# Kernel optimization log

Measured on AMD Instinct MI355X. Metric: run time of the kernel, lower is better.

## Reference

```python
import jax, jax.numpy as jnp
import numpy as np

N_GROUPS = 4


def setup_inputs() -> dict:
    key = jax.random.key(0)
    k1, k2 = jax.random.split(key)
    x = jax.random.normal(k1, (64, 256, 32, 32), dtype=jnp.float32)
    # codebook: (group_size, num_embeddings) = (256 // 4, 512), torch.rand init
    weight = jax.random.uniform(k2, (64, 512), dtype=jnp.float32)
    return {"x": x, "weight": weight}


def _group_quantize(xg, emb):
    # xg: (B, g, H, W), emb: (g, K)
    # squared Euclidean distance; argmin is identical to argmin of torch.norm
    d2 = (jnp.sum(xg * xg, axis=1)[..., None]
          - 2.0 * jnp.einsum('bghw,gk->bhwk', xg, emb)
          + jnp.sum(emb * emb, axis=0))        # (B, H, W, K)
    argmin = jnp.argmin(d2, axis=-1)            # (B, H, W)
    result = jnp.transpose(emb.T[argmin], (0, 3, 1, 2))  # (B, g, H, W)
    return result, argmin


def reference(x, weight):
    B, D, H, W = x.shape
    g = D // N_GROUPS
    results = []
    argmins = []
    for i in range(N_GROUPS):  # fixed small structural loop
        r, a = _group_quantize(x[:, i * g:(i + 1) * g], weight)
        results.append(r)
        argmins.append(a)
    result = jnp.concatenate(results, axis=1) / jnp.sqrt(jnp.float32(N_GROUPS))
    argmins = jnp.stack(argmins, axis=1)  # (B, n_groups, H, W)
    return result, argmins
```

## Files before the change

kernel.cpp:

```cpp
#include <hip/hip_runtime.h>
#include <float.h>

#define KCODES 512
#define GDIM 64
#define TAU 4.0e-3f

typedef __attribute__((ext_vector_type(8))) short short8;
typedef __attribute__((ext_vector_type(4))) float floatx4;


__device__ __forceinline__ void bf16split(float x, short& hi, short& lo) {
    unsigned u = __float_as_uint(x);
    unsigned h = (u + 0x7fffu + ((u >> 16) & 1u)) >> 16;
    hi = (short)h;
    float hf = __uint_as_float(h << 16);
    float l = x - hf;
    unsigned ul = __float_as_uint(l);
    lo = (short)((ul + 0x7fffu + ((ul >> 16) & 1u)) >> 16);
}

__device__ __forceinline__ void gload_lds16(const void* g, void* l) {
    __builtin_amdgcn_global_load_lds(
        (const __attribute__((address_space(1))) void*)g,
        (__attribute__((address_space(3))) void*)l, 16, 0, 0);
}

__launch_bounds__(256)
__global__ void prep_kernel(const float* __restrict__ w,
                            float* __restrict__ embT,
                            float* __restrict__ e2,
                            double* __restrict__ e2d,
                            short* __restrict__ emb_hi,
                            short* __restrict__ emb_lo) {
    int t = blockIdx.x * 256 + threadIdx.x;
    int k = t >> 6;
    int g = t & 63;
    float v = w[(size_t)g * KCODES + k];
    embT[(size_t)k * GDIM + g] = v;
    short h, l; bf16split(-2.0f * v, h, l);
    emb_hi[(size_t)k * GDIM + g] = h;
    emb_lo[(size_t)k * GDIM + g] = l;
    float s = v * v;
    double sd = (double)v * (double)v;
#pragma unroll
    for (int off = 32; off > 0; off >>= 1) {
        s  += __shfl_xor(s, off, 64);
        sd += __shfl_xor(sd, off, 64);
    }
    if (g == 0) { e2[k] = s; e2d[k] = sd; }
}

__launch_bounds__(1024, 4)
__global__ void vq_kernel(const float* __restrict__ x,
                          const float* __restrict__ embT,
                          const float* __restrict__ e2,
                          const double* __restrict__ e2d,
                          const short* __restrict__ emb_hi,
                          const short* __restrict__ emb_lo,
                          float* __restrict__ out_res,
                          float* __restrict__ out_arg) {
    __shared__ short s_hi[512 * 64];
    __shared__ short s_lo[512 * 64];
    __shared__ float s_e2[512];
    __shared__ int   s_arg[512];
    __shared__ float s_fixx[16][64];
    __shared__ int   s_flags[512];
    __shared__ int   s_nflag;

    const int t = threadIdx.x;
    const int wid = t >> 6;
    const int lane = t & 63;
    const int q = lane >> 4;
    const int c = lane & 15;
    const int blk = blockIdx.x;
    const int grp = blk >> 7;
    const int rem = blk & 127;
    const int b = rem >> 1;
    const int half = rem & 1;
    const int hw0 = half * 512 + wid * 32;

    if (t == 0) s_nflag = 0;

#pragma unroll
    for (int i = 0; i < 4; ++i) {
        int r = i * 16 + wid;
        int srcRow = r * 8 + (lane >> 3);
        int srcOff = srcRow * 64 + (((lane & 7) ^ (lane >> 3)) << 3);
        gload_lds16(emb_hi + srcOff, &s_hi[r * 512]);
        gload_lds16(emb_lo + srcOff, &s_lo[r * 512]);
    }
    if (t < 512) s_e2[t] = e2[t];

    const float* xbase = x + (size_t)b * 262144 + (size_t)grp * 65536 + hw0;
    short8 ahi[2][2], alo[2][2];
#pragma unroll
    for (int mt = 0; mt < 2; ++mt)
#pragma unroll
        for (int kt = 0; kt < 2; ++kt) {
#pragma unroll
            for (int j = 0; j < 8; ++j) {
                float xv = xbase[(kt * 32 + q * 8 + j) * 1024 + mt * 16 + c];
                short h, l; bf16split(xv, h, l);
                ahi[mt][kt][j] = h; alo[mt][kt][j] = l;
            }
        }

    float best[2][4], sec[2][4]; int arg[2][4];
#pragma unroll
    for (int mt = 0; mt < 2; ++mt)
#pragma unroll
        for (int r = 0; r < 4; ++r) { best[mt][r] = FLT_MAX; sec[mt][r] = FLT_MAX; arg[mt][r] = 0; }

    const int obase = c * 64 + ((q ^ (c & 7)) << 3);

    __syncthreads();

#pragma unroll 4
    for (int nt = 0; nt < 32; ++nt) {
        const int o = nt * 1024 + obase;
        short8 bh0 = *(const short8*)&s_hi[o];
        short8 bh1 = *(const short8*)&s_hi[o ^ 32];
        short8 bl0 = *(const short8*)&s_lo[o];
        short8 bl1 = *(const short8*)&s_lo[o ^ 32];
        float se2 = s_e2[nt * 16 + c];
#pragma unroll
        for (int mt = 0; mt < 2; ++mt) {
            floatx4 a4 = (floatx4){se2, se2, se2, se2};
            a4 = __builtin_amdgcn_mfma_f32_16x16x32_bf16(alo[mt][0], bh0, a4, 0, 0, 0);
            a4 = __builtin_amdgcn_mfma_f32_16x16x32_bf16(ahi[mt][0], bl0, a4, 0, 0, 0);
            a4 = __builtin_amdgcn_mfma_f32_16x16x32_bf16(ahi[mt][0], bh0, a4, 0, 0, 0);
            a4 = __builtin_amdgcn_mfma_f32_16x16x32_bf16(alo[mt][1], bh1, a4, 0, 0, 0);
            a4 = __builtin_amdgcn_mfma_f32_16x16x32_bf16(ahi[mt][1], bl1, a4, 0, 0, 0);
            a4 = __builtin_amdgcn_mfma_f32_16x16x32_bf16(ahi[mt][1], bh1, a4, 0, 0, 0);
#pragma unroll
            for (int r = 0; r < 4; ++r) {
                float s = a4[r];
                float bo = best[mt][r];
                best[mt][r] = fminf(bo, s);
                arg[mt][r]  = (s < bo) ? nt : arg[mt][r];
                sec[mt][r]  = __builtin_amdgcn_fmed3f(bo, sec[mt][r], s);
            }
        }
    }

#pragma unroll
    for (int mt = 0; mt < 2; ++mt)
#pragma unroll
        for (int r = 0; r < 4; ++r) {
            float b_ = best[mt][r], s_ = sec[mt][r];
            int n_ = arg[mt][r] * 16 + c;
#pragma unroll
            for (int sh = 1; sh < 16; sh <<= 1) {
                float ob = __shfl_xor(b_, sh, 64);
                float os = __shfl_xor(s_, sh, 64);
                int   on = __shfl_xor(n_, sh, 64);
                float bo = b_;
                b_ = fminf(bo, ob);
                n_ = (ob < bo) ? on : n_;
                s_ = fminf(fminf(s_, os), fmaxf(bo, ob));
            }
            if (c == 0) {
                int p = mt * 16 + q * 4 + r;
                s_arg[wid * 32 + p] = n_;
                if (s_ - b_ <= TAU) {
                    int slot = atomicAdd(&s_nflag, 1);
                    s_flags[slot] = hw0 + p;
                }
            }
        }

    {
        int p = lane & 31, gi = lane >> 5;
        int ac = s_arg[wid * 32 + p];
        const float* ev = embT + (size_t)ac * GDIM;
        float* rp = out_res + (size_t)b * 262144 + (size_t)grp * 65536 + hw0 + p;
#pragma unroll
        for (int it = 0; it < 32; ++it) {
            int g = it * 2 + gi;
            rp[(size_t)g * 1024] = ev[g] * 0.5f;
        }
    }

    __syncthreads();
    if (t < 512)
        out_arg[(size_t)b * 4096 + (size_t)grp * 1024 + half * 512 + t] =
            (float)s_arg[t];
    __syncthreads();

    const int nf = s_nflag;
    for (int f = wid; f < nf; f += 16) {
        const int hwa = s_flags[f];
        s_fixx[wid][lane] =
            x[(size_t)b * 262144 + (size_t)grp * 65536 + (size_t)lane * 1024 + hwa];
        asm volatile("s_waitcnt lgkmcnt(0)" ::: "memory");

        double bd = DBL_MAX; int bk = 0;
        for (int m = 0; m < KCODES / 64; ++m) {
            const int k = lane + m * 64;
            const float* er = embT + (size_t)k * GDIM;
            double dot = 0.0;
#pragma unroll
            for (int g = 0; g < GDIM; g += 4) {
                float4 e4 = *(const float4*)(er + g);
                float4 xv = *(const float4*)&s_fixx[wid][g];
                dot += (double)xv.x * (double)e4.x;
                dot += (double)xv.y * (double)e4.y;
                dot += (double)xv.z * (double)e4.z;
                dot += (double)xv.w * (double)e4.w;
            }
            double s = e2d[k] - 2.0 * dot;
            if (s < bd) { bd = s; bk = k; }
        }
        for (int off = 32; off > 0; off >>= 1) {
            double od = __shfl_down(bd, off, 64);
            int    ok = __shfl_down(bk, off, 64);
            if (od < bd || (od == bd && ok < bk)) { bd = od; bk = ok; }
        }
        bk = __shfl(bk, 0, 64);

        if (lane == 0)
            out_arg[(size_t)b * 4096 + (size_t)grp * 1024 + hwa] = (float)bk;
        out_res[(size_t)b * 262144 + (size_t)grp * 65536 + (size_t)lane * 1024 + hwa] =
            embT[(size_t)bk * GDIM + lane] * 0.5f;
    }
}

extern "C" void kernel_launch(void* const* d_in, const int* in_sizes, int n_in,
                              void* d_out, int out_size, void* d_ws, size_t ws_size,
                              hipStream_t stream) {
    const float* x = (const float*)d_in[0];
    const float* w = (const float*)d_in[1];
    float* out_res = (float*)d_out;
    float* out_arg = (float*)d_out + 16777216;

    float*    embT   = (float*)d_ws;
    float*    e2     = embT + 32768;
    double*   e2d    = (double*)((char*)d_ws + (size_t)33280 * 4);
    short*    emb_hi = (short*)((float*)d_ws + 34304);
    short*    emb_lo = (short*)((float*)d_ws + 50688);

    prep_kernel<<<128, 256, 0, stream>>>(w, embT, e2, e2d, emb_hi, emb_lo);
    vq_kernel<<<512, 1024, 0, stream>>>(x, embT, e2, e2d, emb_hi, emb_lo,
                                        out_res, out_arg);
}
```

Before: 248.6 us.

## Stream codebook through double-buffered LDS chunks with smaller 256-thread blocks

The kernel no longer loads the whole 128KB bf16 hi/lo codebook into LDS per block. It uses 256-thread blocks that stream 64-code chunks through a double-buffered LDS tile, prefetching the next chunk asynchronously while computing the current one. This shrinks LDS per block so more blocks can be resident and overlaps codebook loads with MFMA work. In exchange it adds a barrier per chunk, quadruples the grid, and makes each block reload the codebook, raising L2 traffic.

```diff
diff --git a/kernel.cpp b/kernel.cpp
--- a/kernel.cpp
+++ b/kernel.cpp
@@ -50,7 +50,7 @@
     if (g == 0) { e2[k] = s; e2d[k] = sd; }
 }
 
-__launch_bounds__(1024, 4)
+__launch_bounds__(256, 1)
 __global__ void vq_kernel(const float* __restrict__ x,
                           const float* __restrict__ embT,
                           const float* __restrict__ e2,
@@ -59,12 +59,12 @@
                           const short* __restrict__ emb_lo,
                           float* __restrict__ out_res,
                           float* __restrict__ out_arg) {
-    __shared__ short s_hi[512 * 64];
-    __shared__ short s_lo[512 * 64];
+    __shared__ short s_hi[2][64 * 64];
+    __shared__ short s_lo[2][64 * 64];
     __shared__ float s_e2[512];
-    __shared__ int   s_arg[512];
-    __shared__ float s_fixx[16][64];
-    __shared__ int   s_flags[512];
+    __shared__ int   s_arg[128];
+    __shared__ float s_fixx[4][64];
+    __shared__ int   s_flags[128];
     __shared__ int   s_nflag;
 
     const int t = threadIdx.x;
@@ -73,25 +73,35 @@
     const int q = lane >> 4;
     const int c = lane & 15;
     const int blk = blockIdx.x;
-    const int grp = blk >> 7;
-    const int rem = blk & 127;
-    const int b = rem >> 1;
-    const int half = rem & 1;
-    const int hw0 = half * 512 + wid * 32;
+    const int grp = blk >> 9;
+    const int posbase = ((blk & 511) << 7) + wid * 32;
+    const int b = posbase >> 10;
+    const int hwb = posbase & 1023;
 
     if (t == 0) s_nflag = 0;
 
-#pragma unroll
-    for (int i = 0; i < 4; ++i) {
-        int r = i * 16 + wid;
-        int srcRow = r * 8 + (lane >> 3);
-        int srcOff = srcRow * 64 + (((lane & 7) ^ (lane >> 3)) << 3);
-        gload_lds16(emb_hi + srcOff, &s_hi[r * 512]);
-        gload_lds16(emb_lo + srcOff, &s_lo[r * 512]);
-    }
-    if (t < 512) s_e2[t] = e2[t];
-
-    const float* xbase = x + (size_t)b * 262144 + (size_t)grp * 65536 + hw0;
+    const int rA = wid * 16 + (lane >> 3);
+    const int rB = rA + 8;
+    const int uA = (lane & 7) ^ (lane >> 3);
+    const int srcA = rA * 64 + uA * 8;
+    const int srcB = rB * 64 + uA * 8;
+
+#define PREFETCH(CH, BUF)                                                      \
+    {                                                                          \
+        const short* gh_ = emb_hi + (size_t)(CH) * 4096;                       \
+        const short* gl_ = emb_lo + (size_t)(CH) * 4096;                       \
+        gload_lds16(gh_ + srcA, &s_hi[BUF][wid * 1024]);                       \
+        gload_lds16(gh_ + srcB, &s_hi[BUF][wid * 1024 + 512]);                 \
+        gload_lds16(gl_ + srcA, &s_lo[BUF][wid * 1024]);                       \
+        gload_lds16(gl_ + srcB, &s_lo[BUF][wid * 1024 + 512]);                 \
+    }
+
+    PREFETCH(0, 0);
+    s_e2[t] = e2[t];
+    s_e2[t + 256] = e2[t + 256];
+
+    const float* xbase = x + (size_t)b * 262144 + (size_t)grp * 65536 + hwb;
+
     short8 ahi[2][2], alo[2][2];
 #pragma unroll
     for (int mt = 0; mt < 2; ++mt)
@@ -111,44 +121,53 @@
 #pragma unroll
         for (int r = 0; r < 4; ++r) { best[mt][r] = FLT_MAX; sec[mt][r] = FLT_MAX; arg[mt][r] = 0; }
 
-    const int obase = c * 64 + ((q ^ (c & 7)) << 3);
+    const int p8 = (q ^ (c & 7)) << 3;
 
     __syncthreads();
 
-#pragma unroll 4
-    for (int nt = 0; nt < 32; ++nt) {
-        const int o = nt * 1024 + obase;
-        short8 bh0 = *(const short8*)&s_hi[o];
-        short8 bh1 = *(const short8*)&s_hi[o ^ 32];
-        short8 bl0 = *(const short8*)&s_lo[o];
-        short8 bl1 = *(const short8*)&s_lo[o ^ 32];
-        float se2 = s_e2[nt * 16 + c];
-#pragma unroll
-        for (int mt = 0; mt < 2; ++mt) {
-            floatx4 a4 = (floatx4){se2, se2, se2, se2};
-            a4 = __builtin_amdgcn_mfma_f32_16x16x32_bf16(alo[mt][0], bh0, a4, 0, 0, 0);
-            a4 = __builtin_amdgcn_mfma_f32_16x16x32_bf16(ahi[mt][0], bl0, a4, 0, 0, 0);
-            a4 = __builtin_amdgcn_mfma_f32_16x16x32_bf16(ahi[mt][0], bh0, a4, 0, 0, 0);
-            a4 = __builtin_amdgcn_mfma_f32_16x16x32_bf16(alo[mt][1], bh1, a4, 0, 0, 0);
-            a4 = __builtin_amdgcn_mfma_f32_16x16x32_bf16(ahi[mt][1], bl1, a4, 0, 0, 0);
-            a4 = __builtin_amdgcn_mfma_f32_16x16x32_bf16(ahi[mt][1], bh1, a4, 0, 0, 0);
-#pragma unroll
-            for (int r = 0; r < 4; ++r) {
-                float s = a4[r];
-                float bo = best[mt][r];
-                best[mt][r] = fminf(bo, s);
-                arg[mt][r]  = (s < bo) ? nt : arg[mt][r];
-                sec[mt][r]  = __builtin_amdgcn_fmed3f(bo, sec[mt][r], s);
-            }
-        }
+    int cur = 0;
+    for (int ch = 0; ch < 8; ++ch) {
+        if (ch < 7) PREFETCH(ch + 1, cur ^ 1);
+        const int C0 = ch * 64;
+
+#pragma unroll
+        for (int nt = 0; nt < 4; ++nt) {
+            const int o = (nt * 16 + c) * 64 + p8;
+            short8 bh0 = *(const short8*)&s_hi[cur][o];
+            short8 bh1 = *(const short8*)&s_hi[cur][o ^ 32];
+            short8 bl0 = *(const short8*)&s_lo[cur][o];
+            short8 bl1 = *(const short8*)&s_lo[cur][o ^ 32];
+            const float se2 = s_e2[C0 + nt * 16 + c];
+            const int   n   = C0 + nt * 16 + c;
+#pragma unroll
+            for (int mt = 0; mt < 2; ++mt) {
+                floatx4 a4 = (floatx4){se2, se2, se2, se2};
+                a4 = __builtin_amdgcn_mfma_f32_16x16x32_bf16(alo[mt][0], bh0, a4, 0, 0, 0);
+                a4 = __builtin_amdgcn_mfma_f32_16x16x32_bf16(ahi[mt][0], bl0, a4, 0, 0, 0);
+                a4 = __builtin_amdgcn_mfma_f32_16x16x32_bf16(ahi[mt][0], bh0, a4, 0, 0, 0);
+                a4 = __builtin_amdgcn_mfma_f32_16x16x32_bf16(alo[mt][1], bh1, a4, 0, 0, 0);
+                a4 = __builtin_amdgcn_mfma_f32_16x16x32_bf16(ahi[mt][1], bl1, a4, 0, 0, 0);
+                a4 = __builtin_amdgcn_mfma_f32_16x16x32_bf16(ahi[mt][1], bh1, a4, 0, 0, 0);
+#pragma unroll
+                for (int r = 0; r < 4; ++r) {
+                    float s = a4[r];
+                    float bo = best[mt][r];
+                    best[mt][r] = fminf(bo, s);
+                    arg[mt][r]  = (s < bo) ? n : arg[mt][r];
+                    sec[mt][r]  = __builtin_amdgcn_fmed3f(bo, sec[mt][r], s);
+                }
+            }
+        }
+
+        __syncthreads();
+        cur ^= 1;
     }
 
 #pragma unroll
     for (int mt = 0; mt < 2; ++mt)
 #pragma unroll
         for (int r = 0; r < 4; ++r) {
-            float b_ = best[mt][r], s_ = sec[mt][r];
-            int n_ = arg[mt][r] * 16 + c;
+            float b_ = best[mt][r], s_ = sec[mt][r]; int n_ = arg[mt][r];
 #pragma unroll
             for (int sh = 1; sh < 16; sh <<= 1) {
                 float ob = __shfl_xor(b_, sh, 64);
@@ -164,7 +183,7 @@
                 s_arg[wid * 32 + p] = n_;
                 if (s_ - b_ <= TAU) {
                     int slot = atomicAdd(&s_nflag, 1);
-                    s_flags[slot] = hw0 + p;
+                    s_flags[slot] = wid * 32 + p;
                 }
             }
         }
@@ -173,7 +192,7 @@
         int p = lane & 31, gi = lane >> 5;
         int ac = s_arg[wid * 32 + p];
         const float* ev = embT + (size_t)ac * GDIM;
-        float* rp = out_res + (size_t)b * 262144 + (size_t)grp * 65536 + hw0 + p;
+        float* rp = out_res + (size_t)b * 262144 + (size_t)grp * 65536 + hwb + p;
 #pragma unroll
         for (int it = 0; it < 32; ++it) {
             int g = it * 2 + gi;
@@ -182,16 +201,21 @@
     }
 
     __syncthreads();
-    if (t < 512)
-        out_arg[(size_t)b * 4096 + (size_t)grp * 1024 + half * 512 + t] =
+    if (t < 128) {
+        int bp = ((blk & 511) << 7) + t;
+        out_arg[(size_t)(bp >> 10) * 4096 + (size_t)grp * 1024 + (bp & 1023)] =
             (float)s_arg[t];
+    }
     __syncthreads();
 
     const int nf = s_nflag;
-    for (int f = wid; f < nf; f += 16) {
+    for (int f = wid; f < nf; f += 4) {
         const int hwa = s_flags[f];
+        const int pos = ((blk & 511) << 7) + hwa;
+        const int fb = pos >> 10;
+        const int sidx = pos & 1023;
         s_fixx[wid][lane] =
-            x[(size_t)b * 262144 + (size_t)grp * 65536 + (size_t)lane * 1024 + hwa];
+            x[(size_t)fb * 262144 + (size_t)grp * 65536 + (size_t)lane * 1024 + sidx];
         asm volatile("s_waitcnt lgkmcnt(0)" ::: "memory");
 
         double bd = DBL_MAX; int bk = 0;
@@ -219,10 +243,11 @@
         bk = __shfl(bk, 0, 64);
 
         if (lane == 0)
-            out_arg[(size_t)b * 4096 + (size_t)grp * 1024 + hwa] = (float)bk;
-        out_res[(size_t)b * 262144 + (size_t)grp * 65536 + (size_t)lane * 1024 + hwa] =
+            out_arg[(size_t)fb * 4096 + (size_t)grp * 1024 + sidx] = (float)bk;
+        out_res[(size_t)fb * 262144 + (size_t)grp * 65536 + (size_t)lane * 1024 + sidx] =
             embT[(size_t)bk * GDIM + lane] * 0.5f;
     }
+#undef PREFETCH
 }
 
 extern "C" void kernel_launch(void* const* d_in, const int* in_sizes, int n_in,
@@ -240,6 +265,6 @@
     short*    emb_lo = (short*)((float*)d_ws + 50688);
 
     prep_kernel<<<128, 256, 0, stream>>>(w, embT, e2, e2d, emb_hi, emb_lo);
-    vq_kernel<<<512, 1024, 0, stream>>>(x, embT, e2, e2d, emb_hi, emb_lo,
+    vq_kernel<<<2048, 256, 0, stream>>>(x, embT, e2, e2d, emb_hi, emb_lo,
                                         out_res, out_arg);
 }
```

Result: faster. 219.0 us (-11.9%).
